# Kernel tuning notes

Hardware: AMD Instinct MI355X
Metric: run time of the kernel (lower is better)

## Reference

```python
import jax, jax.numpy as jnp
import numpy as np

N_NODES = 50000


def _gcn_conv(x, src, dst, norm, W, b):
    # x: [N, F_in], src/dst: [E+N] (self loops included), norm: [E+N]
    h = x @ W                                   # [N, F_out]
    msg = h[src] * norm[:, None]                # [E+N, F_out] gather + scale
    out = jax.ops.segment_sum(msg, dst, num_segments=N_NODES)  # scatter-add
    return out + b


def _norm_coeffs(edge_index, n_nodes):
    # PyG GCNConv: add self loops, deg over dst (col), norm = d^-1/2[src]*d^-1/2[dst]
    loops = jnp.arange(n_nodes, dtype=edge_index.dtype)
    src = jnp.concatenate([edge_index[0], loops])
    dst = jnp.concatenate([edge_index[1], loops])
    deg = jax.ops.segment_sum(jnp.ones_like(dst, dtype=jnp.float32), dst,
                              num_segments=n_nodes)
    dinv = jnp.where(deg > 0, jax.lax.rsqrt(jnp.maximum(deg, 1.0)), 0.0)
    norm = dinv[src] * dinv[dst]
    return src, dst, norm


def setup_inputs() -> dict:
    key = jax.random.key(0)
    ks = jax.random.split(key, 8)
    F_in, F_hid, E = 128, 128, 600000
    x = jax.random.normal(ks[0], (N_NODES, F_in), dtype=jnp.float32)
    edge_index = jax.random.randint(ks[1], (2, E), 0, N_NODES, dtype=jnp.int32)
    s1 = 1.0 / np.sqrt(F_in)
    s2 = 1.0 / np.sqrt(F_hid)
    W1 = jax.random.uniform(ks[2], (F_in, F_hid), jnp.float32, -s1, s1)
    b1 = jnp.zeros((F_hid,), jnp.float32)
    W2 = jax.random.uniform(ks[3], (F_hid, F_hid), jnp.float32, -s2, s2)
    b2 = jnp.zeros((F_hid,), jnp.float32)
    W3 = jax.random.uniform(ks[4], (F_hid, F_hid), jnp.float32, -s2, s2)
    b3 = jnp.zeros((F_hid,), jnp.float32)
    return {"x": x, "edge_index": edge_index,
            "W1": W1, "b1": b1, "W2": W2, "b2": b2, "W3": W3, "b3": b3}


def reference(x, edge_index, W1, b1, W2, b2, W3, b3):
    src, dst, norm = _norm_coeffs(edge_index, N_NODES)
    h = jax.nn.relu(_gcn_conv(x, src, dst, norm, W1, b1))
    h = jax.nn.relu(_gcn_conv(h, src, dst, norm, W2, b2))
    h = _gcn_conv(h, src, dst, norm, W3, b3)
    # original forward returns (x, h) with x rebound to h (identical arrays)
    return (h, h)
```

## Files before the change

kernel.cpp:

```cpp
#include <hip/hip_runtime.h>

#define NNODES 50000
#define FDIM 128
#define KELL 40

typedef float f4 __attribute__((ext_vector_type(4)));
typedef float f2 __attribute__((ext_vector_type(2)));
typedef short short8 __attribute__((ext_vector_type(8)));
typedef uint uint4v __attribute__((ext_vector_type(4)));
typedef unsigned short ushortt;

__device__ __forceinline__ void split2(float x0, float x1, unsigned& hi, unsigned& lo) {
    unsigned u0 = __float_as_uint(x0), u1 = __float_as_uint(x1);
    unsigned h0 = u0 & 0xffff0000u, h1 = u1 & 0xffff0000u;
    hi = h1 | (h0 >> 16);
    float l0 = x0 - __uint_as_float(h0);
    float l1 = x1 - __uint_as_float(h1);
    lo = (__float_as_uint(l1) & 0xffff0000u) | (__float_as_uint(l0) >> 16);
}

__device__ __forceinline__ unsigned pack2(float lo, float hi) {
    unsigned ul = __float_as_uint(lo);
    unsigned uh = __float_as_uint(hi);
    ul += 0x7fffu + ((ul >> 16) & 1u);
    uh += 0x7fffu + ((uh >> 16) & 1u);
    return (ul >> 16) | (uh & 0xffff0000u);
}

__device__ __forceinline__ f4 dlo(uint4v v) {
    f4 r;
    r.x = __uint_as_float(v.x << 16);
    r.y = __uint_as_float(v.y << 16);
    r.z = __uint_as_float(v.z << 16);
    r.w = __uint_as_float(v.w << 16);
    return r;
}
__device__ __forceinline__ f4 dhi(uint4v v) {
    f4 r;
    r.x = __uint_as_float(v.x & 0xffff0000u);
    r.y = __uint_as_float(v.y & 0xffff0000u);
    r.z = __uint_as_float(v.z & 0xffff0000u);
    r.w = __uint_as_float(v.w & 0xffff0000u);
    return r;
}

__device__ __forceinline__ void prepw_body(const float* __restrict__ W,
                                           unsigned* __restrict__ dh, int p) {
    unsigned* dl = dh + 8192;
    int jp = p & 3;
    int l = (p >> 2) & 63;
    int st = p >> 8;
    int s = st >> 3, t = st & 7;
    int k0 = ((l >> 4) << 3) + (jp << 1) + (s << 5);
    int n = (t << 4) + (l & 15);
    float x0 = W[k0 * 128 + n];
    float x1 = W[(k0 + 1) * 128 + n];
    unsigned hi, lo;
    split2(x0, x1, hi, lo);
    dh[p] = hi;
    dl[p] = lo;
}

#define NB_PREP 96
#define NB_ZERO 196

__global__ __launch_bounds__(256) void k_pre(const float* __restrict__ W1,
                                             const float* __restrict__ W2,
                                             const float* __restrict__ W3,
                                             unsigned* __restrict__ wpk,
                                             int* __restrict__ fill) {
    int bid = blockIdx.x;
    int tid = threadIdx.x;
    if (bid < NB_PREP) {
        int y = bid >> 5;
        const float* W = (y == 0) ? W1 : (y == 1) ? W2 : W3;
        prepw_body(W, wpk + (size_t)y * 16384, (bid & 31) * 256 + tid);
    } else {
        int i = (bid - NB_PREP) * 256 + tid;
        if (i < NNODES) fill[i] = 0;
    }
}

__device__ __forceinline__ void fill_body(const int* __restrict__ src,
                                          const int* __restrict__ dst,
                                          int* __restrict__ fill,
                                          ushortt* __restrict__ col, int E, int i) {
    if (i >= E) return;
    int d = dst[i];
    int s = src[i];
    int slot = atomicAdd(&fill[d], 1);
    if (slot < KELL) col[d * KELL + slot] = (ushortt)s;
}

__device__ __forceinline__ void gemm1_body(const float* __restrict__ A,
                                           const unsigned* __restrict__ wsrc,
                                           unsigned* __restrict__ H, int nrows,
                                           int bid, int tid) {
    int w = tid >> 6, l = tid & 63;
    int m16 = l & 15, q = l >> 4;
    int rbase = bid * 64 + w * 16;
    int row = rbase + m16;
    int rowc = row > nrows - 1 ? nrows - 1 : row;

    union u8 { unsigned u[4]; uint4v uv; short8 v; };
    u8 ah[4], al[4];
    const f4* A4 = (const f4*)A;
#pragma unroll
    for (int s = 0; s < 4; ++s) {
        f4 a0 = A4[(size_t)rowc * 32 + s * 8 + q * 2];
        f4 a1 = A4[(size_t)rowc * 32 + s * 8 + q * 2 + 1];
        split2(a0.x, a0.y, ah[s].u[0], al[s].u[0]);
        split2(a0.z, a0.w, ah[s].u[1], al[s].u[1]);
        split2(a1.x, a1.y, ah[s].u[2], al[s].u[2]);
        split2(a1.z, a1.w, ah[s].u[3], al[s].u[3]);
    }

    f4 acc[8];
#pragma unroll
    for (int t = 0; t < 8; ++t) acc[t] = (f4)0.0f;

    const uint4v* wg4 = (const uint4v*)wsrc;
#pragma unroll
    for (int s = 0; s < 4; ++s) {
#pragma unroll
        for (int t = 0; t < 8; ++t) {
            u8 bh, bl;
            bh.uv = wg4[(s * 8 + t) * 64 + l];
            bl.uv = wg4[2048 + (s * 8 + t) * 64 + l];
            acc[t] = __builtin_amdgcn_mfma_f32_16x16x32_bf16(ah[s].v, bh.v, acc[t], 0, 0, 0);
            acc[t] = __builtin_amdgcn_mfma_f32_16x16x32_bf16(al[s].v, bh.v, acc[t], 0, 0, 0);
            acc[t] = __builtin_amdgcn_mfma_f32_16x16x32_bf16(ah[s].v, bl.v, acc[t], 0, 0, 0);
        }
    }

#pragma unroll
    for (int up = 0; up < 4; ++up) {
#pragma unroll
        for (int r = 0; r < 4; ++r) {
            int rr = rbase + q * 4 + r;
            if (rr < nrows)
                H[(size_t)rr * 64 + up * 16 + m16] =
                    pack2(acc[2 * up][r], acc[2 * up + 1][r]);
        }
    }
}

__global__ __launch_bounds__(256, 4) void k_fillgemm(const float* __restrict__ x,
                                                     const int* __restrict__ src,
                                                     const int* __restrict__ dst,
                                                     int* __restrict__ fill,
                                                     ushortt* __restrict__ col,
                                                     int E, int gb,
                                                     const unsigned* __restrict__ wpk,
                                                     unsigned* __restrict__ H) {
    int bid = blockIdx.x;
    int tid = threadIdx.x;
    if (bid < gb) {
        gemm1_body(x, wpk, H, NNODES, bid, tid);
    } else {
        fill_body(src, dst, fill, col, E, (bid - gb) * 256 + tid);
    }
}

__device__ __forceinline__ void gather16(const unsigned* __restrict__ hpk,
                                         const int* __restrict__ fillv,
                                         const ushortt* __restrict__ colu,
                                         const float* __restrict__ bias,
                                         int n, int sl, int gb16,
                                         f4& olo, f4& ohi) {
    int deg = fillv[n];
    int c = deg < KELL ? deg : KELL;
    float di = rsqrtf(1.0f + (float)deg);
    const uint4v* h4 = (const uint4v*)hpk;
    uint4v sq = h4[(size_t)n * 16 + sl];
    f4 alo = di * dlo(sq);
    f4 ahi = di * dhi(sq);
    int beg = n * KELL;
#pragma unroll 1
    for (int b = 0; b < c; b += 16) {
        int cb = c - b;
        if (cb > 16) cb = 16;
        int cv = 0;
        float wv = 0.0f;
        if (sl < cb) {
            cv = colu[beg + b + sl];
            wv = rsqrtf(1.0f + (float)fillv[cv]);
        }
        int j = 0;
#pragma unroll 1
        for (; j + 8 <= cb; j += 8) {
            int s0 = __shfl(cv, gb16 + j);
            int s1 = __shfl(cv, gb16 + j + 1);
            int s2 = __shfl(cv, gb16 + j + 2);
            int s3 = __shfl(cv, gb16 + j + 3);
            int s4 = __shfl(cv, gb16 + j + 4);
            int s5 = __shfl(cv, gb16 + j + 5);
            int s6 = __shfl(cv, gb16 + j + 6);
            int s7 = __shfl(cv, gb16 + j + 7);
            float w0 = __shfl(wv, gb16 + j);
            float w1 = __shfl(wv, gb16 + j + 1);
            float w2 = __shfl(wv, gb16 + j + 2);
            float w3 = __shfl(wv, gb16 + j + 3);
            float w4 = __shfl(wv, gb16 + j + 4);
            float w5 = __shfl(wv, gb16 + j + 5);
            float w6 = __shfl(wv, gb16 + j + 6);
            float w7 = __shfl(wv, gb16 + j + 7);
            uint4v v0 = h4[(size_t)s0 * 16 + sl];
            uint4v v1 = h4[(size_t)s1 * 16 + sl];
            uint4v v2 = h4[(size_t)s2 * 16 + sl];
            uint4v v3 = h4[(size_t)s3 * 16 + sl];
            uint4v v4 = h4[(size_t)s4 * 16 + sl];
            uint4v v5 = h4[(size_t)s5 * 16 + sl];
            uint4v v6 = h4[(size_t)s6 * 16 + sl];
            uint4v v7 = h4[(size_t)s7 * 16 + sl];
            alo += w0 * dlo(v0); ahi += w0 * dhi(v0);
            alo += w1 * dlo(v1); ahi += w1 * dhi(v1);
            alo += w2 * dlo(v2); ahi += w2 * dhi(v2);
            alo += w3 * dlo(v3); ahi += w3 * dhi(v3);
            alo += w4 * dlo(v4); ahi += w4 * dhi(v4);
            alo += w5 * dlo(v5); ahi += w5 * dhi(v5);
            alo += w6 * dlo(v6); ahi += w6 * dhi(v6);
            alo += w7 * dlo(v7); ahi += w7 * dhi(v7);
        }
#pragma unroll 1
        for (; j + 4 <= cb; j += 4) {
            int s0 = __shfl(cv, gb16 + j);
            int s1 = __shfl(cv, gb16 + j + 1);
            int s2 = __shfl(cv, gb16 + j + 2);
            int s3 = __shfl(cv, gb16 + j + 3);
            float w0 = __shfl(wv, gb16 + j);
            float w1 = __shfl(wv, gb16 + j + 1);
            float w2 = __shfl(wv, gb16 + j + 2);
            float w3 = __shfl(wv, gb16 + j + 3);
            uint4v v0 = h4[(size_t)s0 * 16 + sl];
            uint4v v1 = h4[(size_t)s1 * 16 + sl];
            uint4v v2 = h4[(size_t)s2 * 16 + sl];
            uint4v v3 = h4[(size_t)s3 * 16 + sl];
            alo += w0 * dlo(v0); ahi += w0 * dhi(v0);
            alo += w1 * dlo(v1); ahi += w1 * dhi(v1);
            alo += w2 * dlo(v2); ahi += w2 * dhi(v2);
            alo += w3 * dlo(v3); ahi += w3 * dhi(v3);
        }
#pragma unroll 1
        for (; j < cb; ++j) {
            int s = __shfl(cv, gb16 + j);
            float wgt = __shfl(wv, gb16 + j);
            uint4v v = h4[(size_t)s * 16 + sl];
            alo += wgt * dlo(v);
            ahi += wgt * dhi(v);
        }
    }
    int u = sl >> 2;
    int c0 = u * 32 + (sl & 3) * 4;
    f4 blo = *(const f4*)(bias + c0);
    f4 bhi = *(const f4*)(bias + c0 + 16);
    olo = di * alo + blo;
    ohi = di * ahi + bhi;
}

__global__ __launch_bounds__(128, 4) void k_fused(const unsigned* __restrict__ hin,
                                                  const int* __restrict__ fill,
                                                  const ushortt* __restrict__ colu,
                                                  const float* __restrict__ bias,
                                                  const unsigned* __restrict__ wsrc,
                                                  unsigned* __restrict__ hout) {
    __shared__ float As[16][132];
    int tid = threadIdx.x;
    int w = tid >> 6, l = tid & 63;
    int g = l >> 4, sl = l & 15, gb16 = g * 16;
    int nbase = blockIdx.x * 16;
    int u = sl >> 2;
    int c0 = u * 32 + (sl & 3) * 4;

#pragma unroll 1
    for (int it = 0; it < 2; ++it) {
        int rl = w * 8 + it * 4 + g;
        int n = nbase + rl;
        f4 olo, ohi;
        gather16(hin, fill, colu, bias, n, sl, gb16, olo, ohi);
        olo.x = fmaxf(olo.x, 0.0f); olo.y = fmaxf(olo.y, 0.0f);
        olo.z = fmaxf(olo.z, 0.0f); olo.w = fmaxf(olo.w, 0.0f);
        ohi.x = fmaxf(ohi.x, 0.0f); ohi.y = fmaxf(ohi.y, 0.0f);
        ohi.z = fmaxf(ohi.z, 0.0f); ohi.w = fmaxf(ohi.w, 0.0f);
        *(f4*)&As[rl][c0] = olo;
        *(f4*)&As[rl][c0 + 16] = ohi;
    }
    __syncthreads();

    int m16 = l & 15, q = l >> 4;
    union u8 { unsigned u[4]; uint4v uv; short8 v; };
    u8 ah[4], al[4];
#pragma unroll
    for (int s = 0; s < 4; ++s) {
        f4 a0 = *(const f4*)&As[m16][s * 32 + q * 8];
        f4 a1 = *(const f4*)&As[m16][s * 32 + q * 8 + 4];
        split2(a0.x, a0.y, ah[s].u[0], al[s].u[0]);
        split2(a0.z, a0.w, ah[s].u[1], al[s].u[1]);
        split2(a1.x, a1.y, ah[s].u[2], al[s].u[2]);
        split2(a1.z, a1.w, ah[s].u[3], al[s].u[3]);
    }

    f4 acc[4];
#pragma unroll
    for (int tt = 0; tt < 4; ++tt) acc[tt] = (f4)0.0f;

    const uint4v* wg4 = (const uint4v*)wsrc;
#pragma unroll
    for (int s = 0; s < 4; ++s) {
#pragma unroll
        for (int tt = 0; tt < 4; ++tt) {
            int t = w * 4 + tt;
            u8 bh, bl;
            bh.uv = wg4[(s * 8 + t) * 64 + l];
            bl.uv = wg4[2048 + (s * 8 + t) * 64 + l];
            acc[tt] = __builtin_amdgcn_mfma_f32_16x16x32_bf16(ah[s].v, bh.v, acc[tt], 0, 0, 0);
            acc[tt] = __builtin_amdgcn_mfma_f32_16x16x32_bf16(al[s].v, bh.v, acc[tt], 0, 0, 0);
            acc[tt] = __builtin_amdgcn_mfma_f32_16x16x32_bf16(ah[s].v, bl.v, acc[tt], 0, 0, 0);
        }
    }

#pragma unroll
    for (int p = 0; p < 2; ++p) {
#pragma unroll
        for (int r = 0; r < 4; ++r) {
            int rr = nbase + q * 4 + r;
            hout[(size_t)rr * 64 + (2 * w + p) * 16 + m16] =
                pack2(acc[2 * p][r], acc[2 * p + 1][r]);
        }
    }
}

__global__ __launch_bounds__(256, 4) void k_agg(const unsigned* __restrict__ hpk,
                                                const int* __restrict__ fill,
                                                const ushortt* __restrict__ colu,
                                                const float* __restrict__ bias,
                                                float* __restrict__ out,
                                                float* __restrict__ out2) {
    int gw = (blockIdx.x * 256 + threadIdx.x) >> 6;
    int l = threadIdx.x & 63;
    int g = l >> 4, sl = l & 15, gb16 = g * 16;
    int n = gw * 4 + g;

    f4 olo, ohi;
    gather16(hpk, fill, colu, bias, n, sl, gb16, olo, ohi);

    int u = sl >> 2;
    int c0 = u * 32 + (sl & 3) * 4;
    float* orow = out + (size_t)n * FDIM;
    *(f4*)(orow + c0) = olo;
    *(f4*)(orow + c0 + 16) = ohi;
    float* orow2 = out2 + (size_t)n * FDIM;
    *(f4*)(orow2 + c0) = olo;
    *(f4*)(orow2 + c0 + 16) = ohi;
}

extern "C" void kernel_launch(void* const* d_in, const int* in_sizes, int n_in,
                              void* d_out, int out_size, void* d_ws, size_t ws_size,
                              hipStream_t stream) {
    const float* x  = (const float*)d_in[0];
    const int*   ei = (const int*)d_in[1];
    const float* W1 = (const float*)d_in[2];
    const float* b1 = (const float*)d_in[3];
    const float* W2 = (const float*)d_in[4];
    const float* b2 = (const float*)d_in[5];
    const float* W3 = (const float*)d_in[6];
    const float* b3 = (const float*)d_in[7];
    int E = in_sizes[1] / 2;
    const int* srcp = ei;
    const int* dstp = ei + E;
    float* outf = (float*)d_out;

    unsigned* hpkA = (unsigned*)d_ws;
    int*      fill = (int*)(hpkA + (size_t)NNODES * 64);
    ushortt*  colu = (ushortt*)(fill + NNODES);
    unsigned* wpk  = (unsigned*)(colu + (size_t)NNODES * KELL);
    unsigned* hpkB = (unsigned*)outf;

    int eb = (E + 255) / 256;
    int gb = (NNODES + 63) / 64;
    int fb = NNODES / 16;
    int ab = NNODES / 16;

    k_pre<<<NB_PREP + NB_ZERO, 256, 0, stream>>>(W1, W2, W3, wpk, fill);
    k_fillgemm<<<gb + eb, 256, 0, stream>>>(x, srcp, dstp, fill, colu, E, gb,
                                            wpk, hpkA);
    k_fused<<<fb, 128, 0, stream>>>(hpkA, fill, colu, b1, wpk + 16384, hpkB);
    k_fused<<<fb, 128, 0, stream>>>(hpkB, fill, colu, b2, wpk + 32768, hpkA);
    k_agg<<<ab, 256, 0, stream>>>(hpkA, fill, colu, b3, outf,
                                  outf + (size_t)NNODES * FDIM);
}
```

Baseline: 225.8 us.

## Split fused gather+GEMM into column-chunked aggregation and separate GEMM kernels

Replaces the fused aggregate-then-MFMA kernels with separate passes. A column-chunked aggregation kernel processes the feature dimension in 8 chunks, each thread loading one packed word per neighbor, so each chunk's slice of H is small enough to stay cache-resident across blocks. A standalone GEMM kernel then consumes the fp32 intermediate. This trades extra launches and an fp32 round trip through global memory (into the second output half) for better cache locality during the random gathers.

```diff
diff --git a/kernel.cpp b/kernel.cpp
--- a/kernel.cpp
+++ b/kernel.cpp
@@ -3,9 +3,10 @@
 #define NNODES 50000
 #define FDIM 128
 #define KELL 40
+#define NCH 8
+#define NBC 1563
 
 typedef float f4 __attribute__((ext_vector_type(4)));
-typedef float f2 __attribute__((ext_vector_type(2)));
 typedef short short8 __attribute__((ext_vector_type(8)));
 typedef uint uint4v __attribute__((ext_vector_type(4)));
 typedef unsigned short ushortt;
@@ -25,23 +26,6 @@
     ul += 0x7fffu + ((ul >> 16) & 1u);
     uh += 0x7fffu + ((uh >> 16) & 1u);
     return (ul >> 16) | (uh & 0xffff0000u);
-}
-
-__device__ __forceinline__ f4 dlo(uint4v v) {
-    f4 r;
-    r.x = __uint_as_float(v.x << 16);
-    r.y = __uint_as_float(v.y << 16);
-    r.z = __uint_as_float(v.z << 16);
-    r.w = __uint_as_float(v.w << 16);
-    return r;
-}
-__device__ __forceinline__ f4 dhi(uint4v v) {
-    f4 r;
-    r.x = __uint_as_float(v.x & 0xffff0000u);
-    r.y = __uint_as_float(v.y & 0xffff0000u);
-    r.z = __uint_as_float(v.z & 0xffff0000u);
-    r.w = __uint_as_float(v.w & 0xffff0000u);
-    return r;
 }
 
 __device__ __forceinline__ void prepw_body(const float* __restrict__ W,
@@ -162,24 +146,28 @@
     }
 }
 
-__device__ __forceinline__ void gather16(const unsigned* __restrict__ hpk,
-                                         const int* __restrict__ fillv,
-                                         const ushortt* __restrict__ colu,
-                                         const float* __restrict__ bias,
-                                         int n, int sl, int gb16,
-                                         f4& olo, f4& ohi) {
+__global__ __launch_bounds__(256, 4) void k_gemm(const float* __restrict__ A,
+                                                 const unsigned* __restrict__ wsrc,
+                                                 unsigned* __restrict__ H) {
+    gemm1_body(A, wsrc, H, NNODES, blockIdx.x, threadIdx.x);
+}
+
+__device__ __forceinline__ void cagg_node(const unsigned* __restrict__ hpk,
+                                          const int* __restrict__ fillv,
+                                          const ushortt* __restrict__ colu,
+                                          int n, int sl, int gb8, int wi,
+                                          float& olo, float& ohi, float& dio) {
     int deg = fillv[n];
     int c = deg < KELL ? deg : KELL;
     float di = rsqrtf(1.0f + (float)deg);
-    const uint4v* h4 = (const uint4v*)hpk;
-    uint4v sq = h4[(size_t)n * 16 + sl];
-    f4 alo = di * dlo(sq);
-    f4 ahi = di * dhi(sq);
+    unsigned sw = hpk[(size_t)n * 64 + wi];
+    float alo = di * __uint_as_float(sw << 16);
+    float ahi = di * __uint_as_float(sw & 0xffff0000u);
     int beg = n * KELL;
 #pragma unroll 1
-    for (int b = 0; b < c; b += 16) {
+    for (int b = 0; b < c; b += 8) {
         int cb = c - b;
-        if (cb > 16) cb = 16;
+        if (cb > 8) cb = 8;
         int cv = 0;
         float wv = 0.0f;
         if (sl < cb) {
@@ -189,169 +177,137 @@
         int j = 0;
 #pragma unroll 1
         for (; j + 8 <= cb; j += 8) {
-            int s0 = __shfl(cv, gb16 + j);
-            int s1 = __shfl(cv, gb16 + j + 1);
-            int s2 = __shfl(cv, gb16 + j + 2);
-            int s3 = __shfl(cv, gb16 + j + 3);
-            int s4 = __shfl(cv, gb16 + j + 4);
-            int s5 = __shfl(cv, gb16 + j + 5);
-            int s6 = __shfl(cv, gb16 + j + 6);
-            int s7 = __shfl(cv, gb16 + j + 7);
-            float w0 = __shfl(wv, gb16 + j);
-            float w1 = __shfl(wv, gb16 + j + 1);
-            float w2 = __shfl(wv, gb16 + j + 2);
-            float w3 = __shfl(wv, gb16 + j + 3);
-            float w4 = __shfl(wv, gb16 + j + 4);
-            float w5 = __shfl(wv, gb16 + j + 5);
-            float w6 = __shfl(wv, gb16 + j + 6);
-            float w7 = __shfl(wv, gb16 + j + 7);
-            uint4v v0 = h4[(size_t)s0 * 16 + sl];
-            uint4v v1 = h4[(size_t)s1 * 16 + sl];
-            uint4v v2 = h4[(size_t)s2 * 16 + sl];
-            uint4v v3 = h4[(size_t)s3 * 16 + sl];
-            uint4v v4 = h4[(size_t)s4 * 16 + sl];
-            uint4v v5 = h4[(size_t)s5 * 16 + sl];
-            uint4v v6 = h4[(size_t)s6 * 16 + sl];
-            uint4v v7 = h4[(size_t)s7 * 16 + sl];
-            alo += w0 * dlo(v0); ahi += w0 * dhi(v0);
-            alo += w1 * dlo(v1); ahi += w1 * dhi(v1);
-            alo += w2 * dlo(v2); ahi += w2 * dhi(v2);
-            alo += w3 * dlo(v3); ahi += w3 * dhi(v3);
-            alo += w4 * dlo(v4); ahi += w4 * dhi(v4);
-            alo += w5 * dlo(v5); ahi += w5 * dhi(v5);
-            alo += w6 * dlo(v6); ahi += w6 * dhi(v6);
-            alo += w7 * dlo(v7); ahi += w7 * dhi(v7);
+            int s0 = __shfl(cv, gb8 + j);
+            int s1 = __shfl(cv, gb8 + j + 1);
+            int s2 = __shfl(cv, gb8 + j + 2);
+            int s3 = __shfl(cv, gb8 + j + 3);
+            int s4 = __shfl(cv, gb8 + j + 4);
+            int s5 = __shfl(cv, gb8 + j + 5);
+            int s6 = __shfl(cv, gb8 + j + 6);
+            int s7 = __shfl(cv, gb8 + j + 7);
+            float w0 = __shfl(wv, gb8 + j);
+            float w1 = __shfl(wv, gb8 + j + 1);
+            float w2 = __shfl(wv, gb8 + j + 2);
+            float w3 = __shfl(wv, gb8 + j + 3);
+            float w4 = __shfl(wv, gb8 + j + 4);
+            float w5 = __shfl(wv, gb8 + j + 5);
+            float w6 = __shfl(wv, gb8 + j + 6);
+            float w7 = __shfl(wv, gb8 + j + 7);
+            unsigned v0 = hpk[(size_t)s0 * 64 + wi];
+            unsigned v1 = hpk[(size_t)s1 * 64 + wi];
+            unsigned v2 = hpk[(size_t)s2 * 64 + wi];
+            unsigned v3 = hpk[(size_t)s3 * 64 + wi];
+            unsigned v4 = hpk[(size_t)s4 * 64 + wi];
+            unsigned v5 = hpk[(size_t)s5 * 64 + wi];
+            unsigned v6 = hpk[(size_t)s6 * 64 + wi];
+            unsigned v7 = hpk[(size_t)s7 * 64 + wi];
+            alo += w0 * __uint_as_float(v0 << 16);
+            ahi += w0 * __uint_as_float(v0 & 0xffff0000u);
+            alo += w1 * __uint_as_float(v1 << 16);
+            ahi += w1 * __uint_as_float(v1 & 0xffff0000u);
+            alo += w2 * __uint_as_float(v2 << 16);
+            ahi += w2 * __uint_as_float(v2 & 0xffff0000u);
+            alo += w3 * __uint_as_float(v3 << 16);
+            ahi += w3 * __uint_as_float(v3 & 0xffff0000u);
+            alo += w4 * __uint_as_float(v4 << 16);
+            ahi += w4 * __uint_as_float(v4 & 0xffff0000u);
+            alo += w5 * __uint_as_float(v5 << 16);
+            ahi += w5 * __uint_as_float(v5 & 0xffff0000u);
+            alo += w6 * __uint_as_float(v6 << 16);
+            ahi += w6 * __uint_as_float(v6 & 0xffff0000u);
+            alo += w7 * __uint_as_float(v7 << 16);
+            ahi += w7 * __uint_as_float(v7 & 0xffff0000u);
         }
 #pragma unroll 1
         for (; j + 4 <= cb; j += 4) {
-            int s0 = __shfl(cv, gb16 + j);
-            int s1 = __shfl(cv, gb16 + j + 1);
-            int s2 = __shfl(cv, gb16 + j + 2);
-            int s3 = __shfl(cv, gb16 + j + 3);
-            float w0 = __shfl(wv, gb16 + j);
-            float w1 = __shfl(wv, gb16 + j + 1);
-            float w2 = __shfl(wv, gb16 + j + 2);
-            float w3 = __shfl(wv, gb16 + j + 3);
-            uint4v v0 = h4[(size_t)s0 * 16 + sl];
-            uint4v v1 = h4[(size_t)s1 * 16 + sl];
-            uint4v v2 = h4[(size_t)s2 * 16 + sl];
-            uint4v v3 = h4[(size_t)s3 * 16 + sl];
-            alo += w0 * dlo(v0); ahi += w0 * dhi(v0);
-            alo += w1 * dlo(v1); ahi += w1 * dhi(v1);
-            alo += w2 * dlo(v2); ahi += w2 * dhi(v2);
-            alo += w3 * dlo(v3); ahi += w3 * dhi(v3);
+            int s0 = __shfl(cv, gb8 + j);
+            int s1 = __shfl(cv, gb8 + j + 1);
+            int s2 = __shfl(cv, gb8 + j + 2);
+            int s3 = __shfl(cv, gb8 + j + 3);
+            float w0 = __shfl(wv, gb8 + j);
+            float w1 = __shfl(wv, gb8 + j + 1);
+            float w2 = __shfl(wv, gb8 + j + 2);
+            float w3 = __shfl(wv, gb8 + j + 3);
+            unsigned v0 = hpk[(size_t)s0 * 64 + wi];
+            unsigned v1 = hpk[(size_t)s1 * 64 + wi];
+            unsigned v2 = hpk[(size_t)s2 * 64 + wi];
+            unsigned v3 = hpk[(size_t)s3 * 64 + wi];
+            alo += w0 * __uint_as_float(v0 << 16);
+            ahi += w0 * __uint_as_float(v0 & 0xffff0000u);
+            alo += w1 * __uint_as_float(v1 << 16);
+            ahi += w1 * __uint_as_float(v1 & 0xffff0000u);
+            alo += w2 * __uint_as_float(v2 << 16);
+            ahi += w2 * __uint_as_float(v2 & 0xffff0000u);
+            alo += w3 * __uint_as_float(v3 << 16);
+            ahi += w3 * __uint_as_float(v3 & 0xffff0000u);
         }
 #pragma unroll 1
         for (; j < cb; ++j) {
-            int s = __shfl(cv, gb16 + j);
-            float wgt = __shfl(wv, gb16 + j);
-            uint4v v = h4[(size_t)s * 16 + sl];
-            alo += wgt * dlo(v);
-            ahi += wgt * dhi(v);
-        }
-    }
-    int u = sl >> 2;
-    int c0 = u * 32 + (sl & 3) * 4;
-    f4 blo = *(const f4*)(bias + c0);
-    f4 bhi = *(const f4*)(bias + c0 + 16);
-    olo = di * alo + blo;
-    ohi = di * ahi + bhi;
-}
-
-__global__ __launch_bounds__(128, 4) void k_fused(const unsigned* __restrict__ hin,
-                                                  const int* __restrict__ fill,
-                                                  const ushortt* __restrict__ colu,
-                                                  const float* __restrict__ bias,
-                                                  const unsigned* __restrict__ wsrc,
-                                                  unsigned* __restrict__ hout) {
-    __shared__ float As[16][132];
+            int s = __shfl(cv, gb8 + j);
+            float wgt = __shfl(wv, gb8 + j);
+            unsigned v = hpk[(size_t)s * 64 + wi];
+            alo += wgt * __uint_as_float(v << 16);
+            ahi += wgt * __uint_as_float(v & 0xffff0000u);
+        }
+    }
+    olo = alo;
+    ohi = ahi;
+    dio = di;
+}
+
+__global__ __launch_bounds__(256) void k_cagg(const unsigned* __restrict__ hin,
+                                              const int* __restrict__ fill,
+                                              const ushortt* __restrict__ colu,
+                                              const float* __restrict__ bias,
+                                              float* __restrict__ g) {
+    int bid = blockIdx.x;
+    int p = bid / NBC;
+    int nb = bid - p * NBC;
     int tid = threadIdx.x;
-    int w = tid >> 6, l = tid & 63;
-    int g = l >> 4, sl = l & 15, gb16 = g * 16;
-    int nbase = blockIdx.x * 16;
-    int u = sl >> 2;
-    int c0 = u * 32 + (sl & 3) * 4;
-
-#pragma unroll 1
-    for (int it = 0; it < 2; ++it) {
-        int rl = w * 8 + it * 4 + g;
-        int n = nbase + rl;
-        f4 olo, ohi;
-        gather16(hin, fill, colu, bias, n, sl, gb16, olo, ohi);
-        olo.x = fmaxf(olo.x, 0.0f); olo.y = fmaxf(olo.y, 0.0f);
-        olo.z = fmaxf(olo.z, 0.0f); olo.w = fmaxf(olo.w, 0.0f);
-        ohi.x = fmaxf(ohi.x, 0.0f); ohi.y = fmaxf(ohi.y, 0.0f);
-        ohi.z = fmaxf(ohi.z, 0.0f); ohi.w = fmaxf(ohi.w, 0.0f);
-        *(f4*)&As[rl][c0] = olo;
-        *(f4*)&As[rl][c0 + 16] = ohi;
-    }
-    __syncthreads();
-
-    int m16 = l & 15, q = l >> 4;
-    union u8 { unsigned u[4]; uint4v uv; short8 v; };
-    u8 ah[4], al[4];
-#pragma unroll
-    for (int s = 0; s < 4; ++s) {
-        f4 a0 = *(const f4*)&As[m16][s * 32 + q * 8];
-        f4 a1 = *(const f4*)&As[m16][s * 32 + q * 8 + 4];
-        split2(a0.x, a0.y, ah[s].u[0], al[s].u[0]);
-        split2(a0.z, a0.w, ah[s].u[1], al[s].u[1]);
-        split2(a1.x, a1.y, ah[s].u[2], al[s].u[2]);
-        split2(a1.z, a1.w, ah[s].u[3], al[s].u[3]);
-    }
-
-    f4 acc[4];
-#pragma unroll
-    for (int tt = 0; tt < 4; ++tt) acc[tt] = (f4)0.0f;
-
-    const uint4v* wg4 = (const uint4v*)wsrc;
-#pragma unroll
-    for (int s = 0; s < 4; ++s) {
-#pragma unroll
-        for (int tt = 0; tt < 4; ++tt) {
-            int t = w * 4 + tt;
-            u8 bh, bl;
-            bh.uv = wg4[(s * 8 + t) * 64 + l];
-            bl.uv = wg4[2048 + (s * 8 + t) * 64 + l];
-            acc[tt] = __builtin_amdgcn_mfma_f32_16x16x32_bf16(ah[s].v, bh.v, acc[tt], 0, 0, 0);
-            acc[tt] = __builtin_amdgcn_mfma_f32_16x16x32_bf16(al[s].v, bh.v, acc[tt], 0, 0, 0);
-            acc[tt] = __builtin_amdgcn_mfma_f32_16x16x32_bf16(ah[s].v, bl.v, acc[tt], 0, 0, 0);
-        }
-    }
-
-#pragma unroll
-    for (int p = 0; p < 2; ++p) {
-#pragma unroll
-        for (int r = 0; r < 4; ++r) {
-            int rr = nbase + q * 4 + r;
-            hout[(size_t)rr * 64 + (2 * w + p) * 16 + m16] =
-                pack2(acc[2 * p][r], acc[2 * p + 1][r]);
-        }
-    }
-}
-
-__global__ __launch_bounds__(256, 4) void k_agg(const unsigned* __restrict__ hpk,
-                                                const int* __restrict__ fill,
-                                                const ushortt* __restrict__ colu,
-                                                const float* __restrict__ bias,
-                                                float* __restrict__ out,
-                                                float* __restrict__ out2) {
-    int gw = (blockIdx.x * 256 + threadIdx.x) >> 6;
-    int l = threadIdx.x & 63;
-    int g = l >> 4, sl = l & 15, gb16 = g * 16;
-    int n = gw * 4 + g;
-
-    f4 olo, ohi;
-    gather16(hpk, fill, colu, bias, n, sl, gb16, olo, ohi);
-
-    int u = sl >> 2;
-    int c0 = u * 32 + (sl & 3) * 4;
-    float* orow = out + (size_t)n * FDIM;
-    *(f4*)(orow + c0) = olo;
-    *(f4*)(orow + c0 + 16) = ohi;
-    float* orow2 = out2 + (size_t)n * FDIM;
-    *(f4*)(orow2 + c0) = olo;
-    *(f4*)(orow2 + c0 + 16) = ohi;
+    int sl = tid & 7;
+    int gb8 = (tid & 63) & ~7;
+    int n = nb * 32 + (tid >> 3);
+    if (n >= NNODES) return;
+    int wi = p * 8 + sl;
+
+    float alo, ahi, di;
+    cagg_node(hin, fill, colu, n, sl, gb8, wi, alo, ahi, di);
+
+    int u = wi >> 4, m = wi & 15;
+    int c0 = u * 32 + m;
+    float r0 = fmaxf(di * alo + bias[c0], 0.0f);
+    float r1 = fmaxf(di * ahi + bias[c0 + 16], 0.0f);
+    g[(size_t)n * FDIM + c0] = r0;
+    g[(size_t)n * FDIM + c0 + 16] = r1;
+}
+
+__global__ __launch_bounds__(256) void k_caggF(const unsigned* __restrict__ hin,
+                                               const int* __restrict__ fill,
+                                               const ushortt* __restrict__ colu,
+                                               const float* __restrict__ bias,
+                                               float* __restrict__ out,
+                                               float* __restrict__ out2) {
+    int bid = blockIdx.x;
+    int p = bid / NBC;
+    int nb = bid - p * NBC;
+    int tid = threadIdx.x;
+    int sl = tid & 7;
+    int gb8 = (tid & 63) & ~7;
+    int n = nb * 32 + (tid >> 3);
+    if (n >= NNODES) return;
+    int wi = p * 8 + sl;
+
+    float alo, ahi, di;
+    cagg_node(hin, fill, colu, n, sl, gb8, wi, alo, ahi, di);
+
+    int u = wi >> 4, m = wi & 15;
+    int c0 = u * 32 + m;
+    float r0 = di * alo + bias[c0];
+    float r1 = di * ahi + bias[c0 + 16];
+    out[(size_t)n * FDIM + c0] = r0;
+    out[(size_t)n * FDIM + c0 + 16] = r1;
+    out2[(size_t)n * FDIM + c0] = r0;
+    out2[(size_t)n * FDIM + c0 + 16] = r1;
 }
 
 extern "C" void kernel_launch(void* const* d_in, const int* in_sizes, int n_in,
@@ -375,17 +331,19 @@
     ushortt*  colu = (ushortt*)(fill + NNODES);
     unsigned* wpk  = (unsigned*)(colu + (size_t)NNODES * KELL);
     unsigned* hpkB = (unsigned*)outf;
+    float*    g    = outf + (size_t)NNODES * FDIM;
 
     int eb = (E + 255) / 256;
     int gb = (NNODES + 63) / 64;
-    int fb = NNODES / 16;
-    int ab = NNODES / 16;
+    int cb = NCH * NBC;
 
     k_pre<<<NB_PREP + NB_ZERO, 256, 0, stream>>>(W1, W2, W3, wpk, fill);
     k_fillgemm<<<gb + eb, 256, 0, stream>>>(x, srcp, dstp, fill, colu, E, gb,
                                             wpk, hpkA);
-    k_fused<<<fb, 128, 0, stream>>>(hpkA, fill, colu, b1, wpk + 16384, hpkB);
-    k_fused<<<fb, 128, 0, stream>>>(hpkB, fill, colu, b2, wpk + 32768, hpkA);
-    k_agg<<<ab, 256, 0, stream>>>(hpkA, fill, colu, b3, outf,
-                                  outf + (size_t)NNODES * FDIM);
-}
+    k_cagg<<<cb, 256, 0, stream>>>(hpkA, fill, colu, b1, g);
+    k_gemm<<<gb, 256, 0, stream>>>(g, wpk + 16384, hpkB);
+    k_cagg<<<cb, 256, 0, stream>>>(hpkB, fill, colu, b2, g);
+    k_gemm<<<gb, 256, 0, stream>>>(g, wpk + 32768, hpkA);
+    k_caggF<<<cb, 256, 0, stream>>>(hpkA, fill, colu, b3, outf,
+                                    outf + (size_t)NNODES * FDIM);
+}
```

Result: slower. 380.8 us (+68.6%).
